# Performance work log

Hardware: AMD Instinct MI355X
Metric: run time of the kernel (lower is better)

The kernel has to match this reference:

```python
import jax, jax.numpy as jnp
import numpy as np

DIM = 768
N_HEADS = 12
HEAD_DIM = DIM // N_HEADS
HIDDEN = int(DIM * 4.0)
B, S = 4, 2048
EPS = 1e-6
SCALE = HEAD_DIM ** -0.5


def layer_norm(x, gamma, beta):
    mu = jnp.mean(x, axis=-1, keepdims=True)
    var = jnp.mean((x - mu) ** 2, axis=-1, keepdims=True)
    return (x - mu) * jax.lax.rsqrt(var + EPS) * gamma + beta


def setup_inputs() -> dict:
    key = jax.random.key(0)
    ks = jax.random.split(key, 8)
    x = jax.random.normal(ks[0], (B, S, DIM), dtype=jnp.float32)
    mask = jax.random.randint(ks[1], (B, 1, S, S), 0, 2, dtype=jnp.int32)
    sd = DIM ** -0.5
    return {
        "x": x,
        "mask": mask,
        "w_qkv": jax.random.normal(ks[2], (DIM, 3 * DIM), dtype=jnp.float32) * sd,
        "b_qkv": jnp.zeros((3 * DIM,), jnp.float32),
        "w_proj": jax.random.normal(ks[3], (DIM, DIM), dtype=jnp.float32) * sd,
        "b_proj": jnp.zeros((DIM,), jnp.float32),
        "g1": jnp.ones((DIM,), jnp.float32),
        "beta1": jnp.zeros((DIM,), jnp.float32),
        "g2": jnp.ones((DIM,), jnp.float32),
        "beta2": jnp.zeros((DIM,), jnp.float32),
        "w1": jax.random.normal(ks[4], (DIM, HIDDEN), dtype=jnp.float32) * sd,
        "b1": jnp.zeros((HIDDEN,), jnp.float32),
        "w2": jax.random.normal(ks[5], (HIDDEN, DIM), dtype=jnp.float32) * (HIDDEN ** -0.5),
        "b2": jnp.zeros((DIM,), jnp.float32),
    }


def reference(x, mask, w_qkv, b_qkv, w_proj, b_proj, g1, beta1, g2, beta2, w1, b1, w2, b2):
    # --- attention branch (pre-LN) ---
    h = layer_norm(x, g1, beta1)
    qkv = h @ w_qkv + b_qkv                              # (B,S,3*DIM)
    qkv = qkv.reshape(B, S, 3, N_HEADS, HEAD_DIM)
    q, k, v = (qkv[:, :, 0], qkv[:, :, 1], qkv[:, :, 2])  # (B,S,H,D)
    # scores: (B,H,S,S) -- materialized like the original
    dp = jnp.einsum("bqhd,bkhd->bhqk", q, k) * SCALE
    dp = jnp.where(mask == 0, jnp.float32(-10000.0), dp)
    attn = jax.nn.softmax(dp, axis=-1)
    wa = jnp.einsum("bhqk,bkhd->bqhd", attn, v).reshape(B, S, DIM)
    x = x + (wa @ w_proj + b_proj)
    # --- MLP branch (pre-LN) ---
    h = layer_norm(x, g2, beta2)
    h = jax.nn.gelu(h @ w1 + b1, approximate=False)
    x = x + (h @ w2 + b2)
    return x
```

## Files before the change

### kernel.cpp

```cpp
#include <hip/hip_runtime.h>
#include <hip/hip_bf16.h>
#include <math.h>

typedef __bf16 bf16;
typedef __bf16 bf16x8 __attribute__((ext_vector_type(8)));
typedef short bf16x4s __attribute__((ext_vector_type(4)));
typedef float f32x4 __attribute__((ext_vector_type(4)));

#define DIM 768
#define NH 12
#define HD 64
#define HID 3072
#define BB 4
#define SS 2048
#define QPRESCALE 0.18033688011112042f

#define MFMA(a, b, c) __builtin_amdgcn_mfma_f32_16x16x32_bf16(a, b, c, 0, 0, 0)
#define MFMA16(a, b, c) \
  __builtin_amdgcn_mfma_f32_16x16x16bf16_1k(a, b, c, 0, 0, 0)

__device__ __forceinline__ void gld16(const void* g, void* l) {
  __builtin_amdgcn_global_load_lds(
      (const __attribute__((address_space(1))) void*)g,
      (__attribute__((address_space(3))) void*)l, 16, 0, 0);
}

__device__ __forceinline__ unsigned pk2(float a, float b) {
  union {
    bf16 h[2];
    unsigned u;
  } t;
  t.h[0] = (bf16)a;
  t.h[1] = (bf16)b;
  return t.u;
}

__global__ __launch_bounds__(256) void castT_all_kernel(
    const float* __restrict__ s0, bf16* __restrict__ d0,
    const float* __restrict__ s1, bf16* __restrict__ d1,
    const float* __restrict__ s2, bf16* __restrict__ d2,
    const float* __restrict__ s3, bf16* __restrict__ d3) {
  __shared__ float tile[32][33];
  int id = blockIdx.x;
  const float* in;
  bf16* out;
  int R, C, loc;
  if (id < 1728) { in = s0; out = d0; R = 768; C = 2304; loc = id; }
  else if (id < 2304) { in = s1; out = d1; R = 768; C = 768; loc = id - 1728; }
  else if (id < 4608) { in = s2; out = d2; R = 768; C = 3072; loc = id - 2304; }
  else { in = s3; out = d3; R = 3072; C = 768; loc = id - 4608; }
  const int cb = C >> 5;
  const int c0 = (loc % cb) * 32, r0 = (loc / cb) * 32;
  const int tx = threadIdx.x & 31, ty = threadIdx.x >> 5;
#pragma unroll
  for (int i = 0; i < 32; i += 8)
    tile[ty + i][tx] = in[(size_t)(r0 + ty + i) * C + c0 + tx];
  __syncthreads();
#pragma unroll
  for (int i = 0; i < 32; i += 8)
    out[(size_t)(c0 + ty + i) * R + r0 + tx] = (bf16)tile[tx][ty + i];
}

__global__ __launch_bounds__(256) void maskbits_kernel(
    const int* __restrict__ mask, unsigned* __restrict__ bits) {
  const int i = blockIdx.x * 256 + threadIdx.x;
  unsigned long long m = __ballot(mask[i] != 0);
  const int lane = threadIdx.x & 63;
  if (lane == 0) bits[i >> 5] = (unsigned)m;
  else if (lane == 32) bits[i >> 5] = (unsigned)(m >> 32);
}

__global__ __launch_bounds__(256) void ln_kernel(
    const float* __restrict__ x, const float* __restrict__ g,
    const float* __restrict__ beta, bf16* __restrict__ out) {
  const int row = blockIdx.x, t = threadIdx.x;
  const float* xr = x + (size_t)row * DIM;
  float v0 = xr[t], v1 = xr[t + 256], v2 = xr[t + 512];
  float s = v0 + v1 + v2;
  float s2 = v0 * v0 + v1 * v1 + v2 * v2;
#pragma unroll
  for (int d = 1; d < 64; d <<= 1) {
    s += __shfl_xor(s, d);
    s2 += __shfl_xor(s2, d);
  }
  __shared__ float red[8];
  const int wv = t >> 6, lane = t & 63;
  if (lane == 0) { red[wv] = s; red[wv + 4] = s2; }
  __syncthreads();
  s = red[0] + red[1] + red[2] + red[3];
  s2 = red[4] + red[5] + red[6] + red[7];
  const float mu = s * (1.0f / DIM);
  const float var = s2 * (1.0f / DIM) - mu * mu;
  const float r = rsqrtf(var + 1e-6f);
  bf16* o = out + (size_t)row * DIM;
  o[t] = (bf16)((v0 - mu) * r * g[t] + beta[t]);
  o[t + 256] = (bf16)((v1 - mu) * r * g[t + 256] + beta[t + 256]);
  o[t + 512] = (bf16)((v2 - mu) * r * g[t + 512] + beta[t + 512]);
}

enum { EPI_QKV = 0, EPI_PROJ = 1, EPI_FFN1 = 2, EPI_FFN2 = 3 };

template <int EPI, int K, int TN>
__global__ __launch_bounds__(256) void gemm_kernel(
    const bf16* __restrict__ A, const bf16* __restrict__ Bt,
    const float* __restrict__ bias, const float* __restrict__ res,
    void* __restrict__ o0, void* __restrict__ o1, void* __restrict__ o2) {
  constexpr int MI = (TN == 128) ? 4 : 2;
  __shared__ bf16 As[128 * 64];
  __shared__ bf16 Bs[TN * 64];
  const int tid = threadIdx.x;
  const int wv = tid >> 6, lane = tid & 63;
  const int quad = lane >> 4, l15 = lane & 15;
  const int lrow = lane >> 3, lcol = lane & 7;
  const int m0 = blockIdx.y * 128, n0 = blockIdx.x * TN;
  const int wm = (TN == 128) ? (wv >> 1) * 64 : wv * 32;
  const int wn = (TN == 128) ? (wv & 1) * 64 : 0;

  f32x4 acc[MI][4] = {};

  const int swz = (lcol ^ lrow) * 8;
  const bf16* Ag = A + (size_t)(m0 + wv * 32 + lrow) * K + swz;
  const bf16* Bg = Bt + (size_t)(n0 + wv * (TN / 4) + lrow) * K + swz;
  bf16* Al = As + (wv * 32) * 64;
  bf16* Bl = Bs + (wv * (TN / 4)) * 64;

  for (int k0 = 0; k0 < K; k0 += 64) {
#pragma unroll
    for (int i = 0; i < 4; i++)
      gld16(Ag + (size_t)(i * 8) * K + k0, Al + i * 8 * 64);
#pragma unroll
    for (int i = 0; i < TN / 32; i++)
      gld16(Bg + (size_t)(i * 8) * K + k0, Bl + i * 8 * 64);
    __syncthreads();
#pragma unroll
    for (int ks = 0; ks < 2; ks++) {
      bf16x8 af[MI], bfr[4];
#pragma unroll
      for (int i = 0; i < MI; i++) {
        const int ra = wm + i * 16 + l15;
        af[i] = *(const bf16x8*)&As[ra * 64 + ((ks * 4 + quad) ^ (ra & 7)) * 8];
      }
#pragma unroll
      for (int i = 0; i < 4; i++) {
        const int rb = wn + i * 16 + l15;
        bfr[i] = *(const bf16x8*)&Bs[rb * 64 + ((ks * 4 + quad) ^ (rb & 7)) * 8];
      }
#pragma unroll
      for (int mi = 0; mi < MI; mi++)
#pragma unroll
        for (int ni = 0; ni < 4; ni++)
          acc[mi][ni] = MFMA(af[mi], bfr[ni], acc[mi][ni]);
    }
    __syncthreads();
  }

#pragma unroll
  for (int mi = 0; mi < MI; mi++) {
#pragma unroll
    for (int ni = 0; ni < 4; ni++) {
      const int n = n0 + wn + ni * 16 + l15;
      const float bv = bias[n];
      const int mb = m0 + wm + mi * 16 + quad * 4;
      float val[4];
#pragma unroll
      for (int r = 0; r < 4; r++) val[r] = acc[mi][ni][r] + bv;
      if (EPI == EPI_QKV) {
        const int which = n / 768;
        const int nn = n - which * 768;
        const int hh = nn >> 6, d = nn & 63;
        const int bb = mb >> 11, s = mb & 2047;
        if (which == 0) {
#pragma unroll
          for (int r = 0; r < 4; r++)
            ((bf16*)o0)[((size_t)(bb * NH + hh) * SS + s + r) * HD + d] =
                (bf16)(val[r] * QPRESCALE);
        } else if (which == 1) {
#pragma unroll
          for (int r = 0; r < 4; r++)
            ((bf16*)o1)[((size_t)(bb * NH + hh) * SS + s + r) * HD + d] =
                (bf16)val[r];
        } else {
          uint2 pv;
          pv.x = pk2(val[0], val[1]);
          pv.y = pk2(val[2], val[3]);
          *(uint2*)&((bf16*)o2)[((size_t)(bb * NH + hh) * HD + d) * SS + s] = pv;
        }
      } else if (EPI == EPI_PROJ) {
#pragma unroll
        for (int r = 0; r < 4; r++)
          ((float*)o0)[(size_t)(mb + r) * DIM + n] =
              res[(size_t)(mb + r) * DIM + n] + val[r];
      } else if (EPI == EPI_FFN1) {
#pragma unroll
        for (int r = 0; r < 4; r++) {
          const float ge =
              0.5f * val[r] * (1.0f + erff(val[r] * 0.70710678118654752f));
          ((bf16*)o0)[(size_t)(mb + r) * HID + n] = (bf16)ge;
        }
      } else {
#pragma unroll
        for (int r = 0; r < 4; r++)
          ((float*)o0)[(size_t)(mb + r) * DIM + n] =
              res[(size_t)(mb + r) * DIM + n] + val[r];
      }
    }
  }
}

__global__ __launch_bounds__(256) void attn_kernel(
    const bf16* __restrict__ q, const bf16* __restrict__ k,
    const bf16* __restrict__ vT, const unsigned* __restrict__ bits,
    bf16* __restrict__ wa) {
  const int b = blockIdx.z, h = blockIdx.y, q0 = blockIdx.x * 128;
  const int tid = threadIdx.x, wv = tid >> 6, lane = tid & 63;
  const int quad = lane >> 4, l15 = lane & 15;
  const int lrow = lane >> 3, lcol = lane & 7;

  __shared__ bf16 Ks[64 * 64];
  __shared__ bf16 Vs[64 * 64];
  __shared__ unsigned lut[32];

  if (tid < 16) {
    lut[2 * tid] =
        ((tid & 1) ? 0xFFFFu : 0u) | ((tid & 2) ? 0xFFFF0000u : 0u);
    lut[2 * tid + 1] =
        ((tid & 4) ? 0xFFFFu : 0u) | ((tid & 8) ? 0xFFFF0000u : 0u);
  }

  const bf16* qbh = q + (size_t)(b * NH + h) * SS * HD;
  const bf16* kbh = k + (size_t)(b * NH + h) * SS * HD;
  const bf16* vbh = vT + (size_t)(b * NH + h) * HD * SS;

  bf16x8 aq[2][2];
#pragma unroll
  for (int mi = 0; mi < 2; mi++)
#pragma unroll
    for (int ks = 0; ks < 2; ks++) {
      const int s = q0 + wv * 32 + mi * 16 + l15;
      aq[mi][ks] = *(const bf16x8*)&qbh[(size_t)s * HD + ks * 32 + quad * 8];
    }

  const unsigned long long* mrow[2];
#pragma unroll
  for (int mi = 0; mi < 2; mi++)
    mrow[mi] = (const unsigned long long*)bits +
               (size_t)(b * SS + q0 + wv * 32 + mi * 16 + l15) * 32;

  f32x4 O[2][4] = {};
  f32x4 lm[2] = {};
  const short oneb = 0x3F80;
  const bf16x4s onesA = {oneb, oneb, oneb, oneb};
  const int swz = (lcol ^ lrow) * 8;

  for (int t = 0; t < SS / 64; ++t) {
    const int s0 = t * 64;
#pragma unroll
    for (int i = 0; i < 2; i++) {
      const int r = wv * 16 + i * 8 + lrow;
      gld16(&kbh[(size_t)(s0 + r) * HD + swz], &Ks[(wv * 16 + i * 8) * 64]);
      gld16(&vbh[(size_t)r * SS + s0 + swz], &Vs[(wv * 16 + i * 8) * 64]);
    }
    const unsigned long long sh0 = mrow[0][t] >> (quad * 4);
    const unsigned long long sh1 = mrow[1][t] >> (quad * 4);
    const unsigned lo0 = (unsigned)sh0, hi0 = (unsigned)(sh0 >> 32);
    const unsigned lo1 = (unsigned)sh1, hi1 = (unsigned)(sh1 >> 32);
    __syncthreads();

#pragma unroll
    for (int ni = 0; ni < 4; ni++) {
      const int rr = ni * 16 + l15;
      const bf16x8 kf0 = *(const bf16x8*)&Ks[rr * 64 + (quad ^ (rr & 7)) * 8];
      const bf16x8 kf1 =
          *(const bf16x8*)&Ks[rr * 64 + ((4 + quad) ^ (rr & 7)) * 8];
      f32x4 a0 = {}, a1 = {};
      a0 = MFMA(kf0, aq[0][0], a0);
      a0 = MFMA(kf1, aq[0][1], a0);
      a1 = MFMA(kf0, aq[1][0], a1);
      a1 = MFMA(kf1, aq[1][1], a1);
      const unsigned nib0 = (ni == 0)   ? (lo0 & 0xF)
                            : (ni == 1) ? ((lo0 >> 16) & 0xF)
                            : (ni == 2) ? (hi0 & 0xF)
                                        : ((hi0 >> 16) & 0xF);
      const unsigned nib1 = (ni == 0)   ? (lo1 & 0xF)
                            : (ni == 1) ? ((lo1 >> 16) & 0xF)
                            : (ni == 2) ? (hi1 & 0xF)
                                        : ((hi1 >> 16) & 0xF);
      const uint2 mw0 = *(const uint2*)&lut[2 * nib0];
      const uint2 mw1 = *(const uint2*)&lut[2 * nib1];
      union {
        unsigned u[2];
        bf16x4s v;
      } p0, p1;
      p0.u[0] = pk2(__builtin_amdgcn_exp2f(a0[0]),
                    __builtin_amdgcn_exp2f(a0[1])) & mw0.x;
      p0.u[1] = pk2(__builtin_amdgcn_exp2f(a0[2]),
                    __builtin_amdgcn_exp2f(a0[3])) & mw0.y;
      p1.u[0] = pk2(__builtin_amdgcn_exp2f(a1[0]),
                    __builtin_amdgcn_exp2f(a1[1])) & mw1.x;
      p1.u[1] = pk2(__builtin_amdgcn_exp2f(a1[2]),
                    __builtin_amdgcn_exp2f(a1[3])) & mw1.y;
      lm[0] = MFMA16(onesA, p0.v, lm[0]);
      lm[1] = MFMA16(onesA, p1.v, lm[1]);
#pragma unroll
      for (int nd = 0; nd < 4; nd++) {
        const int row = nd * 16 + l15;
        const int pc = (ni * 2 + (quad >> 1)) ^ (row & 7);
        const bf16x4s vf =
            *(const bf16x4s*)&Vs[row * 64 + pc * 8 + (quad & 1) * 4];
        O[0][nd] = MFMA16(vf, p0.v, O[0][nd]);
        O[1][nd] = MFMA16(vf, p1.v, O[1][nd]);
      }
    }
    __syncthreads();
  }

#pragma unroll
  for (int mi = 0; mi < 2; mi++) {
    const float rln = __builtin_amdgcn_rcpf(lm[mi][0]);
    const int sq = q0 + wv * 32 + mi * 16 + l15;
    bf16* dst = wa + (size_t)(b * SS + sq) * DIM + h * HD + quad * 4;
#pragma unroll
    for (int nd = 0; nd < 4; nd++) {
      uint2 pv;
      pv.x = pk2(O[mi][nd][0] * rln, O[mi][nd][1] * rln);
      pv.y = pk2(O[mi][nd][2] * rln, O[mi][nd][3] * rln);
      *(uint2*)&dst[nd * 16] = pv;
    }
  }
}

extern "C" void kernel_launch(void* const* d_in, const int* in_sizes, int n_in,
                              void* d_out, int out_size, void* d_ws,
                              size_t ws_size, hipStream_t stream) {
  const float* x = (const float*)d_in[0];
  const int* mask = (const int*)d_in[1];
  const float* w_qkv = (const float*)d_in[2];
  const float* b_qkv = (const float*)d_in[3];
  const float* w_proj = (const float*)d_in[4];
  const float* b_proj = (const float*)d_in[5];
  const float* g1 = (const float*)d_in[6];
  const float* beta1 = (const float*)d_in[7];
  const float* g2 = (const float*)d_in[8];
  const float* beta2 = (const float*)d_in[9];
  const float* w1 = (const float*)d_in[10];
  const float* b1 = (const float*)d_in[11];
  const float* w2 = (const float*)d_in[12];
  const float* b2 = (const float*)d_in[13];
  float* out = (float*)d_out;

  char* p = (char*)d_ws;
  auto alloc = [&](size_t bytes) {
    char* r = p;
    p += (bytes + 1023) & ~(size_t)1023;
    return r;
  };
  bf16* wqkvT = (bf16*)alloc((size_t)2304 * 768 * 2);
  bf16* wprojT = (bf16*)alloc((size_t)768 * 768 * 2);
  bf16* w1T = (bf16*)alloc((size_t)3072 * 768 * 2);
  bf16* w2T = (bf16*)alloc((size_t)768 * 3072 * 2);
  unsigned* bits = (unsigned*)alloc((size_t)BB * SS * 64 * 4);
  bf16* h = (bf16*)alloc((size_t)8192 * 768 * 2);
  bf16* qb = (bf16*)alloc((size_t)8192 * 768 * 2);
  bf16* kb = (bf16*)alloc((size_t)8192 * 768 * 2);
  bf16* vtb = (bf16*)alloc((size_t)8192 * 768 * 2);
  bf16* wab = (bf16*)alloc((size_t)8192 * 768 * 2);
  float* x2 = (float*)alloc((size_t)8192 * 768 * 4);
  bf16* ffn1 = (bf16*)alloc((size_t)8192 * 3072 * 2);

  castT_all_kernel<<<6912, 256, 0, stream>>>(w_qkv, wqkvT, w_proj, wprojT, w1,
                                             w1T, w2, w2T);
  maskbits_kernel<<<(BB * SS * SS) / 256, 256, 0, stream>>>(mask, bits);
  ln_kernel<<<8192, 256, 0, stream>>>(x, g1, beta1, h);
  gemm_kernel<EPI_QKV, 768, 128>
      <<<dim3(2304 / 128, 8192 / 128), 256, 0, stream>>>(h, wqkvT, b_qkv,
                                                         nullptr, qb, kb, vtb);
  attn_kernel<<<dim3(SS / 128, NH, BB), 256, 0, stream>>>(qb, kb, vtb, bits,
                                                          wab);
  gemm_kernel<EPI_PROJ, 768, 64>
      <<<dim3(768 / 64, 8192 / 128), 256, 0, stream>>>(wab, wprojT, b_proj, x,
                                                       x2, nullptr, nullptr);
  ln_kernel<<<8192, 256, 0, stream>>>(x2, g2, beta2, h);
  gemm_kernel<EPI_FFN1, 768, 128>
      <<<dim3(3072 / 128, 8192 / 128), 256, 0, stream>>>(h, w1T, b1, nullptr,
                                                         ffn1, nullptr,
                                                         nullptr);
  gemm_kernel<EPI_FFN2, 3072, 64>
      <<<dim3(768 / 64, 8192 / 128), 256, 0, stream>>>(ffn1, w2T, b2, x2, out,
                                                       nullptr, nullptr);
}
```

Before: 505.1 us.

## Double-buffer GEMM LDS tiles and use 128x64 tiles for all GEMMs

The GEMM kernel now keeps two LDS buffers and issues the async global-to-LDS loads for the next K slice before computing the current one, with a single barrier per iteration. This overlaps memory latency with MFMA work. The 128x128 tile variant is also dropped, so the QKV and FFN1 GEMMs now run with 128x64 tiles and twice as many blocks. That lowers per-block data reuse, and doubling LDS use may reduce occupancy.

```diff
diff --git a/kernel.cpp b/kernel.cpp
--- a/kernel.cpp
+++ b/kernel.cpp
@@ -100,65 +100,71 @@
 
 enum { EPI_QKV = 0, EPI_PROJ = 1, EPI_FFN1 = 2, EPI_FFN2 = 3 };
 
-template <int EPI, int K, int TN>
+template <int EPI, int K>
 __global__ __launch_bounds__(256) void gemm_kernel(
     const bf16* __restrict__ A, const bf16* __restrict__ Bt,
     const float* __restrict__ bias, const float* __restrict__ res,
     void* __restrict__ o0, void* __restrict__ o1, void* __restrict__ o2) {
-  constexpr int MI = (TN == 128) ? 4 : 2;
-  __shared__ bf16 As[128 * 64];
-  __shared__ bf16 Bs[TN * 64];
+  constexpr int NIT = K / 64;
+  __shared__ bf16 As[2][128 * 64];
+  __shared__ bf16 Bs[2][64 * 64];
   const int tid = threadIdx.x;
   const int wv = tid >> 6, lane = tid & 63;
   const int quad = lane >> 4, l15 = lane & 15;
   const int lrow = lane >> 3, lcol = lane & 7;
-  const int m0 = blockIdx.y * 128, n0 = blockIdx.x * TN;
-  const int wm = (TN == 128) ? (wv >> 1) * 64 : wv * 32;
-  const int wn = (TN == 128) ? (wv & 1) * 64 : 0;
-
-  f32x4 acc[MI][4] = {};
+  const int m0 = blockIdx.y * 128, n0 = blockIdx.x * 64;
+  const int wm = wv * 32;
+
+  f32x4 acc[2][4] = {};
 
   const int swz = (lcol ^ lrow) * 8;
   const bf16* Ag = A + (size_t)(m0 + wv * 32 + lrow) * K + swz;
-  const bf16* Bg = Bt + (size_t)(n0 + wv * (TN / 4) + lrow) * K + swz;
-  bf16* Al = As + (wv * 32) * 64;
-  bf16* Bl = Bs + (wv * (TN / 4)) * 64;
-
-  for (int k0 = 0; k0 < K; k0 += 64) {
+  const bf16* Bg = Bt + (size_t)(n0 + wv * 16 + lrow) * K + swz;
+
+  auto stage = [&](int buf, int k0) {
 #pragma unroll
     for (int i = 0; i < 4; i++)
-      gld16(Ag + (size_t)(i * 8) * K + k0, Al + i * 8 * 64);
-#pragma unroll
-    for (int i = 0; i < TN / 32; i++)
-      gld16(Bg + (size_t)(i * 8) * K + k0, Bl + i * 8 * 64);
+      gld16(Ag + (size_t)(i * 8) * K + k0, &As[buf][(wv * 32 + i * 8) * 64]);
+#pragma unroll
+    for (int i = 0; i < 2; i++)
+      gld16(Bg + (size_t)(i * 8) * K + k0,
+            &Bs[buf][(wv * 16 + i * 8) * 64]);
+  };
+
+  stage(0, 0);
+
+  for (int it = 0; it < NIT; ++it) {
     __syncthreads();
+    if (it + 1 < NIT) stage((it + 1) & 1, (it + 1) * 64);
+    const bf16* Ab = As[it & 1];
+    const bf16* Bb = Bs[it & 1];
 #pragma unroll
     for (int ks = 0; ks < 2; ks++) {
-      bf16x8 af[MI], bfr[4];
-#pragma unroll
-      for (int i = 0; i < MI; i++) {
+      bf16x8 af[2], bfr[4];
+#pragma unroll
+      for (int i = 0; i < 2; i++) {
         const int ra = wm + i * 16 + l15;
-        af[i] = *(const bf16x8*)&As[ra * 64 + ((ks * 4 + quad) ^ (ra & 7)) * 8];
+        af[i] = *(const bf16x8*)&Ab[ra * 64 + ((ks * 4 + quad) ^ (ra & 7)) * 8];
       }
 #pragma unroll
       for (int i = 0; i < 4; i++) {
-        const int rb = wn + i * 16 + l15;
-        bfr[i] = *(const bf16x8*)&Bs[rb * 64 + ((ks * 4 + quad) ^ (rb & 7)) * 8];
+        const int rb = i * 16 + l15;
+        bfr[i] =
+            *(const bf16x8*)&Bb[rb * 64 + ((ks * 4 + quad) ^ (rb & 7)) * 8];
       }
 #pragma unroll
-      for (int mi = 0; mi < MI; mi++)
+      for (int mi = 0; mi < 2; mi++)
 #pragma unroll
         for (int ni = 0; ni < 4; ni++)
           acc[mi][ni] = MFMA(af[mi], bfr[ni], acc[mi][ni]);
     }
-    __syncthreads();
-  }
-
-#pragma unroll
-  for (int mi = 0; mi < MI; mi++) {
+  }
+
+#pragma unroll
+  for (int mi = 0; mi < 2; mi++) {
 #pragma unroll
     for (int ni = 0; ni < 4; ni++) {
-      const int n = n0 + wn + ni * 16 + l15;
+      const int n = n0 + ni * 16 + l15;
       const float bv = bias[n];
       const int mb = m0 + wm + mi * 16 + quad * 4;
       float val[4];
@@ -371,20 +377,20 @@
                                              w1T, w2, w2T);
   maskbits_kernel<<<(BB * SS * SS) / 256, 256, 0, stream>>>(mask, bits);
   ln_kernel<<<8192, 256, 0, stream>>>(x, g1, beta1, h);
-  gemm_kernel<EPI_QKV, 768, 128>
-      <<<dim3(2304 / 128, 8192 / 128), 256, 0, stream>>>(h, wqkvT, b_qkv,
-                                                         nullptr, qb, kb, vtb);
+  gemm_kernel<EPI_QKV, 768>
+      <<<dim3(2304 / 64, 8192 / 128), 256, 0, stream>>>(h, wqkvT, b_qkv,
+                                                        nullptr, qb, kb, vtb);
   attn_kernel<<<dim3(SS / 128, NH, BB), 256, 0, stream>>>(qb, kb, vtb, bits,
                                                           wab);
-  gemm_kernel<EPI_PROJ, 768, 64>
+  gemm_kernel<EPI_PROJ, 768>
       <<<dim3(768 / 64, 8192 / 128), 256, 0, stream>>>(wab, wprojT, b_proj, x,
                                                        x2, nullptr, nullptr);
   ln_kernel<<<8192, 256, 0, stream>>>(x2, g2, beta2, h);
-  gemm_kernel<EPI_FFN1, 768, 128>
-      <<<dim3(3072 / 128, 8192 / 128), 256, 0, stream>>>(h, w1T, b1, nullptr,
-                                                         ffn1, nullptr,
-                                                         nullptr);
-  gemm_kernel<EPI_FFN2, 3072, 64>
+  gemm_kernel<EPI_FFN1, 768>
+      <<<dim3(3072 / 64, 8192 / 128), 256, 0, stream>>>(h, w1T, b1, nullptr,
+                                                        ffn1, nullptr,
+                                                        nullptr);
+  gemm_kernel<EPI_FFN2, 3072>
       <<<dim3(768 / 64, 8192 / 128), 256, 0, stream>>>(ffn1, w2T, b2, x2, out,
                                                        nullptr, nullptr);
 }
```

Result: faster. 494.1 us (-2.2%).
